# Kernel tuning notes

Hardware: AMD Instinct MI355X
Metric: run time of the kernel (lower is better)

## Reference

```python
import jax, jax.numpy as jnp
import numpy as np

N_NODES = 100000
SEQ = 16          # spiral length
IN_C = 3
NUM_CLASSES = 12


def _xavier(key, shape):
    fan_out, fan_in = shape
    limit = float(np.sqrt(6.0 / (fan_in + fan_out)))
    return jax.random.uniform(key, shape, jnp.float32, -limit, limit)


def setup_inputs() -> dict:
    key = jax.random.key(0)
    ks = jax.random.split(key, 8)
    x = jax.random.normal(ks[0], (N_NODES, IN_C), jnp.float32)
    indices = jax.random.randint(ks[1], (N_NODES, SEQ), 0, N_NODES, jnp.int64)
    return {
        "x": x,
        "indices": indices,
        "fc0_w": _xavier(ks[2], (16, IN_C)),
        "fc0_b": jnp.zeros((16,), jnp.float32),
        "w1": _xavier(ks[3], (32, 16 * SEQ)),
        "b1": jnp.zeros((32,), jnp.float32),
        "w2": _xavier(ks[4], (64, 32 * SEQ)),
        "b2": jnp.zeros((64,), jnp.float32),
        "w3": _xavier(ks[5], (128, 64 * SEQ)),
        "b3": jnp.zeros((128,), jnp.float32),
        "fc1_w": _xavier(ks[6], (256, 128)),
        "fc1_b": jnp.zeros((256,), jnp.float32),
        "fc2_w": _xavier(ks[7], (NUM_CLASSES, 256)),
        "fc2_b": jnp.zeros((NUM_CLASSES,), jnp.float32),
    }


def _spiral_conv(x, indices, w, b):
    # gather spiral neighborhoods: [N, S, C] -> [N, S*C], then linear
    n = indices.shape[0]
    g = x[indices.reshape(-1)].reshape(n, -1)
    return g @ w.T + b


def reference(x, indices, fc0_w, fc0_b, w1, b1, w2, b2, w3, b3,
              fc1_w, fc1_b, fc2_w, fc2_b):
    h = jax.nn.elu(x @ fc0_w.T + fc0_b)                 # [N, 16]
    h = jax.nn.elu(_spiral_conv(h, indices, w1, b1))    # [N, 32]
    h = jax.nn.elu(_spiral_conv(h, indices, w2, b2))    # [N, 64]
    h = jax.nn.elu(_spiral_conv(h, indices, w3, b3))    # [N, 128]
    h = jax.nn.elu(h @ fc1_w.T + fc1_b)                 # [N, 256]
    # dropout is identity in eval mode
    logits = h @ fc2_w.T + fc2_b                        # [N, num_classes]
    return jax.nn.log_softmax(logits, axis=1)
```

## Files before the change

### kernel.cpp

```cpp
#include <hip/hip_runtime.h>
#include <hip/hip_fp8.h>
#include <math.h>
#include <utility>


typedef __bf16 bf16x8 __attribute__((ext_vector_type(8)));
typedef float f32x16 __attribute__((ext_vector_type(16)));
typedef float f32x2 __attribute__((ext_vector_type(2)));

template <int V> using ic = std::integral_constant<int, V>;

template <typename F, int... Is>
__device__ __forceinline__ void static_for_impl(F&& f, std::integer_sequence<int, Is...>) {
    (f(ic<Is>{}), ...);
}
template <int N_, typename F>
__device__ __forceinline__ void static_for(F&& f) {
    static_for_impl(static_cast<F&&>(f), std::make_integer_sequence<int, N_>{});
}

template <int N_>
__device__ __forceinline__ void wait_vmcnt() {
    static_assert(N_ <= 63, "vmcnt range");
    __builtin_amdgcn_s_waitcnt((N_ & 0xF) | (0x7 << 4) | (0xF << 8) | ((N_ >> 4) << 14));
}

__device__ __forceinline__ void memfence_sched() { __builtin_amdgcn_sched_barrier(0x000F); }

__device__ __forceinline__ float elu_f(float v) { return v > 0.f ? v : expm1f(v); }

__device__ __forceinline__ unsigned char to_fp8(float v) {
    int p = __builtin_amdgcn_cvt_pk_fp8_f32(v, v, 0, false);
    return (unsigned char)p;
}

__device__ __forceinline__ unsigned int pk_bf16(float a, float b) {
    unsigned int r;
    asm("v_cvt_pk_bf16_f32 %0, %1, %2" : "=v"(r) : "v"(a), "v"(b));
    return r;
}

__device__ __forceinline__ bf16x8 dq8(long v) {
    unsigned int lo = (unsigned int)(unsigned long)v;
    unsigned int hi = (unsigned int)((unsigned long)v >> 32);
    f32x2 f0 = __builtin_amdgcn_cvt_pk_f32_fp8((int)lo, false);
    f32x2 f1 = __builtin_amdgcn_cvt_pk_f32_fp8((int)lo, true);
    f32x2 f2 = __builtin_amdgcn_cvt_pk_f32_fp8((int)hi, false);
    f32x2 f3 = __builtin_amdgcn_cvt_pk_f32_fp8((int)hi, true);
    union { unsigned int u[4]; bf16x8 b; } r;
    r.u[0] = pk_bf16(f0[0], f0[1]);
    r.u[1] = pk_bf16(f1[0], f1[1]);
    r.u[2] = pk_bf16(f2[0], f2[1]);
    r.u[3] = pk_bf16(f3[0], f3[1]);
    return r.b;
}

template <int K, int C>
__device__ __forceinline__ void swz_one(const float* __restrict__ src, __bf16* __restrict__ dst, int j)
{
    int col = j / K;
    int k = j & (K - 1);
    int chunk = ((k >> 6) * 8 + ((k & 63) >> 3)) * C + col;
    dst[chunk * 8 + (k & 7)] = (__bf16)src[j];
}

__global__ __launch_bounds__(256) void cvt_swz_kernel(const float* __restrict__ w1,
                                                      const float* __restrict__ w2,
                                                      const float* __restrict__ w3,
                                                      const float* __restrict__ f1,
                                                      const float* __restrict__ f2,
                                                      __bf16* __restrict__ d1,
                                                      __bf16* __restrict__ d2,
                                                      __bf16* __restrict__ d3,
                                                      __bf16* __restrict__ df1,
                                                      __bf16* __restrict__ df2p)
{
    int i = blockIdx.x * 256 + threadIdx.x;
    if (i < 8192)        swz_one<256, 32>(w1, d1, i);
    else if (i < 40960)  swz_one<512, 64>(w2, d2, i - 8192);
    else if (i < 172032) swz_one<1024, 128>(w3, d3, i - 40960);
    else if (i < 204800) swz_one<128, 256>(f1, df1, i - 172032);
    else if (i < 212992) {
        int d = i - 204800;
        int e = d & 7;
        int chunkIdx = d >> 3;
        int col = chunkIdx & 31;
        int q = chunkIdx >> 5;
        int k = (q >> 3) * 64 + (q & 7) * 8 + e;
        df2p[d] = (col < 12) ? (__bf16)f2[col * 256 + k] : (__bf16)0.f;
    }
}

__global__ __launch_bounds__(256) void idxT_kernel(const int* __restrict__ idx,
                                                   int* __restrict__ idxT, int N)
{
    int i = blockIdx.x * 256 + threadIdx.x;
    if (i >= N * 16) return;
    int n = i >> 4, s = i & 15;
    idxT[s * N + n] = idx[i];
}

__global__ __launch_bounds__(256) void fc0_kernel(const float* __restrict__ x,
                                                  const float* __restrict__ w,
                                                  const float* __restrict__ b,
                                                  __bf16* __restrict__ h0, int N)
{
    int n = blockIdx.x * 256 + threadIdx.x;
    if (n >= N) return;
    float x0 = x[n * 3 + 0], x1 = x[n * 3 + 1], x2 = x[n * 3 + 2];
    __bf16 ob[16];
#pragma unroll
    for (int j = 0; j < 16; ++j)
        ob[j] = (__bf16)elu_f(w[j * 3 + 0] * x0 + w[j * 3 + 1] * x1 + w[j * 3 + 2] * x2 + b[j]);
    int4* dst = (int4*)&h0[(size_t)n * 16];
    dst[0] = *(int4*)&ob[0];
    dst[1] = *(int4*)&ob[8];
}

template <int CIN, int S, int COUT_B, int COUT_TOT, int TILE_M, int RW, int CW,
          bool GATHER, bool OUTF8, int MINW, int NN>
__global__ __launch_bounds__(256, MINW) void mfma_layer(const __bf16* __restrict__ hin,
                                                        const int* __restrict__ idxT,
                                                        const __bf16* __restrict__ Wsw,
                                                        const float* __restrict__ bias,
                                                        void* __restrict__ hout)
{
    constexpr int K = CIN * S;
    constexpr int NSTEP = K / 64;
    static_assert(K % 64 == 0, "K%64");
    constexpr int WM = TILE_M / RW;
    constexpr int WN = COUT_B / CW;
    constexpr int MT = WM / 32;
    constexpr int NT = WN / 32;
    constexpr int IPS = GATHER ? (64 / CIN) : 1;
    constexpr int D = WM / 8;
    constexpr int Bn = NT * 4;
    constexpr int I = GATHER ? D : 0;
    constexpr int NBUFS = 3;
    static_assert(RW * CW == 4, "4 waves");
    static_assert(WM == 32 || WM == 64, "1-2 row subtiles per wave");

    constexpr int AB = 4 * NBUFS * WM * 128;
    constexpr int CB = OUTF8 ? TILE_M * (COUT_B + 16) : TILE_M * (COUT_B + 8) * 2;
    constexpr int SH = AB > CB ? AB : CB;
    __shared__ __align__(16) char smem[SH];

    const int tid = threadIdx.x;
    const int lane = tid & 63;
    const int w = tid >> 6;
    const int wr = w / CW;
    const int wc = w % CW;
    const int ml = lane & 31;
    const int kh = lane >> 5;
    const int m0 = blockIdx.x * TILE_M;
    const int col0 = blockIdx.y * COUT_B;
    const int rbase = m0 + wr * WM;

    char* const Aw = smem + w * (NBUFS * WM * 128);

    int ioff[GATHER ? D : 1];
    int koff[GATHER ? D : 1];
    int gmr[GATHER ? 1 : D];
    int coff[GATHER ? 1 : D];
#pragma unroll
    for (int i = 0; i < D; ++i) {
        int r = i * 8 + (lane >> 3);
        int c = (lane & 7) ^ (r & 7);
        int gm = rbase + r; if (gm >= NN) gm = NN - 1;
        if constexpr (GATHER) {
            ioff[i] = ((c * 8) / CIN) * NN + gm;
            koff[i] = (c * 8) & (CIN - 1);
        } else {
            gmr[i] = gm;
            coff[i] = c * 8;
        }
    }

    bf16x8 bfr[2][NT][4];
    int myIdx[GATHER ? 3 : 1][GATHER ? D : 1];

    const __bf16* wlane = Wsw + ((size_t)(col0 + wc * WN + ml) + (size_t)kh * COUT_TOT) * 8;

    auto loadB = [&](auto sc) {
        constexpr int s = decltype(sc)::value;
        if constexpr (s < NSTEP) {
#pragma unroll
            for (int ni = 0; ni < NT; ++ni)
#pragma unroll
                for (int ks = 0; ks < 4; ++ks)
                    bfr[s & 1][ni][ks] = *(const bf16x8*)(wlane
                        + (size_t)(s * 8 + ks * 2) * COUT_TOT * 8 + ni * 32 * 8);
        }
    };
    auto loadIdxS = [&](auto sc) {
        constexpr int s = decltype(sc)::value;
        if constexpr (GATHER && s < NSTEP) {
#pragma unroll
            for (int i = 0; i < D; ++i)
                myIdx[s % 3][i] = idxT[(s * IPS) * NN + ioff[i]];
        }
    };
    auto issueDMA = [&](auto sc) {
        constexpr int s = decltype(sc)::value;
        if constexpr (s < NSTEP) {
            char* base = Aw + (s % NBUFS) * (WM * 128);
#pragma unroll
            for (int i = 0; i < D; ++i) {
                const __bf16* src;
                if constexpr (GATHER)
                    src = hin + (size_t)myIdx[s % 3][i] * CIN + koff[i];
                else
                    src = hin + (size_t)gmr[i] * K + s * 64 + coff[i];
                __builtin_amdgcn_global_load_lds(
                    (const __attribute__((address_space(1))) void*)src,
                    (__attribute__((address_space(3))) void*)(base + i * 1024),
                    16, 0, 0);
            }
        }
    };

    f32x16 acc[MT][NT];
#pragma unroll
    for (int mi = 0; mi < MT; ++mi)
#pragma unroll
        for (int ni = 0; ni < NT; ++ni) { f32x16 z = {}; acc[mi][ni] = z; }

    loadIdxS(ic<0>{});
    loadIdxS(ic<1>{});
    loadIdxS(ic<2>{});
    memfence_sched();
    loadB(ic<0>{});
    memfence_sched();
    issueDMA(ic<0>{});
    memfence_sched();
    issueDMA(ic<1>{});
    memfence_sched();
    loadIdxS(ic<3>{});
    memfence_sched();

    static_for<NSTEP>([&](auto sc) {
        constexpr int s = decltype(sc)::value;
        constexpr int NW = D * (s + 1 < NSTEP) + I * (s + 3 < NSTEP);
        wait_vmcnt<NW>();
        memfence_sched();

        const char* base = Aw + (s % NBUFS) * (WM * 128);
        bf16x8 afr[MT][4];
#pragma unroll
        for (int mi = 0; mi < MT; ++mi)
#pragma unroll
            for (int ks = 0; ks < 4; ++ks) {
                int cb = ks * 2 + kh;
                afr[mi][ks] = *(const bf16x8*)(base + ((mi * 32 + ml) * 8 + (cb ^ (ml & 7))) * 16);
            }
        memfence_sched();

        loadB(ic<s + 1>{});
        memfence_sched();
        issueDMA(ic<s + 2>{});
        memfence_sched();
        loadIdxS(ic<s + 4>{});
        memfence_sched();

#pragma unroll
        for (int ks = 0; ks < 4; ++ks)
#pragma unroll
            for (int mi = 0; mi < MT; ++mi)
#pragma unroll
                for (int ni = 0; ni < NT; ++ni)
                    acc[mi][ni] = __builtin_amdgcn_mfma_f32_32x32x16_bf16(
                        afr[mi][ks], bfr[s & 1][ni][ks], acc[mi][ni], 0, 0, 0);
    });

    __syncthreads();
    if constexpr (OUTF8) {
        unsigned char* Cs8 = (unsigned char*)smem;
        constexpr int LDC8 = COUT_B + 16;
#pragma unroll
        for (int ni = 0; ni < NT; ++ni) {
            const int col = wc * WN + ni * 32 + ml;
            const float bv = bias[col0 + col];
#pragma unroll
            for (int mi = 0; mi < MT; ++mi) {
#pragma unroll
                for (int r = 0; r < 16; ++r) {
                    int row = wr * WM + mi * 32 + ((r & 3) + 8 * (r >> 2) + 4 * kh);
                    Cs8[row * LDC8 + col] = to_fp8(elu_f(acc[mi][ni][r] + bv));
                }
            }
        }
        __syncthreads();
        constexpr int C16 = COUT_B / 16;
#pragma unroll
        for (int j2 = tid; j2 < TILE_M * C16; j2 += 256) {
            int row = j2 / C16, c16 = j2 % C16;
            int gm = m0 + row;
            if (gm < NN)
                *(int4*)((unsigned char*)hout + (size_t)gm * COUT_TOT + col0 + c16 * 16)
                    = *(int4*)&Cs8[row * LDC8 + c16 * 16];
        }
    } else {
        __bf16* Cs = (__bf16*)smem;
        constexpr int LDC = COUT_B + 8;
#pragma unroll
        for (int ni = 0; ni < NT; ++ni) {
            const int col = wc * WN + ni * 32 + ml;
            const float bv = bias[col0 + col];
#pragma unroll
            for (int mi = 0; mi < MT; ++mi) {
#pragma unroll
                for (int r = 0; r < 16; ++r) {
                    int row = wr * WM + mi * 32 + ((r & 3) + 8 * (r >> 2) + 4 * kh);
                    Cs[row * LDC + col] = (__bf16)elu_f(acc[mi][ni][r] + bv);
                }
            }
        }
        __syncthreads();
        constexpr int C8 = COUT_B / 8;
#pragma unroll
        for (int j2 = tid; j2 < TILE_M * C8; j2 += 256) {
            int row = j2 / C8, c8 = j2 % C8;
            int gm = m0 + row;
            if (gm < NN)
                *(int4*)&((__bf16*)hout)[(size_t)gm * COUT_TOT + col0 + c8 * 8] = *(int4*)&Cs[row * LDC + c8 * 8];
        }
    }
}

__global__ __launch_bounds__(256, 3) void mfma3_mixed(const unsigned char* __restrict__ h2f8,
                                                      const int* __restrict__ idxT,
                                                      const __bf16* __restrict__ Wsw,
                                                      const float* __restrict__ bias,
                                                      __bf16* __restrict__ h3)
{
    constexpr int NN = 100000;
    constexpr int NSTEP = 16;
    constexpr int D = 2;
    constexpr int Bn = 8;
    constexpr int I = 2;
    constexpr int NBUFS = 3;
    __shared__ __align__(16) char smem[24576];

    const int tid = threadIdx.x;
    const int lane = tid & 63;
    const int w = tid >> 6;
    const int wr = w >> 1;
    const int wc = w & 1;
    const int ml = lane & 31;
    const int kh = lane >> 5;
    const int m0 = blockIdx.x * 64;
    const int rbase = m0 + wr * 32;

    char* const Aw = smem + w * (NBUFS * 2048);

    int ioff[D], koff[D];
#pragma unroll
    for (int i = 0; i < D; ++i) {
        int r = i * 16 + (lane >> 2);
        int c = (lane & 3) ^ (r & 3) ^ ((r >> 2) & 3);
        int gm = rbase + r; if (gm >= NN) gm = NN - 1;
        ioff[i] = gm;
        koff[i] = c * 16;
    }

    bf16x8 bfr[2][2][4];
    int myIdx[3][D];

    const __bf16* wlane = Wsw + ((size_t)(wc * 64 + ml) + (size_t)kh * 128) * 8;

    auto loadB = [&](auto sc) {
        constexpr int s = decltype(sc)::value;
        if constexpr (s < NSTEP) {
#pragma unroll
            for (int ni = 0; ni < 2; ++ni)
#pragma unroll
                for (int ks = 0; ks < 4; ++ks)
                    bfr[s & 1][ni][ks] = *(const bf16x8*)(wlane
                        + (size_t)(s * 8 + ks * 2) * 128 * 8 + ni * 32 * 8);
        }
    };
    auto loadIdxS = [&](auto sc) {
        constexpr int s = decltype(sc)::value;
        if constexpr (s < NSTEP) {
#pragma unroll
            for (int i = 0; i < D; ++i)
                myIdx[s % 3][i] = idxT[(size_t)s * NN + ioff[i]];
        }
    };
    auto issueDMA = [&](auto sc) {
        constexpr int s = decltype(sc)::value;
        if constexpr (s < NSTEP) {
            char* base = Aw + (s % NBUFS) * 2048;
#pragma unroll
            for (int i = 0; i < D; ++i) {
                const unsigned char* src = h2f8 + (size_t)myIdx[s % 3][i] * 64 + koff[i];
                __builtin_amdgcn_global_load_lds(
                    (const __attribute__((address_space(1))) void*)src,
                    (__attribute__((address_space(3))) void*)(base + i * 1024),
                    16, 0, 0);
            }
        }
    };

    f32x16 acc[2];
    { f32x16 z = {}; acc[0] = z; acc[1] = z; }

    loadIdxS(ic<0>{});
    loadIdxS(ic<1>{});
    loadIdxS(ic<2>{});
    memfence_sched();
    loadB(ic<0>{});
    memfence_sched();
    issueDMA(ic<0>{});
    memfence_sched();
    issueDMA(ic<1>{});
    memfence_sched();
    loadIdxS(ic<3>{});
    memfence_sched();

    static_for<NSTEP>([&](auto sc) {
        constexpr int s = decltype(sc)::value;
        constexpr int NW = (s == 0)
            ? (D * (1 < NSTEP) + I * (3 < NSTEP))
            : (I * (s + 2 < NSTEP) + Bn + D * (s + 1 < NSTEP) + I * (s + 3 < NSTEP));
        wait_vmcnt<NW>();
        memfence_sched();

        const char* base = Aw + (s % NBUFS) * 2048;
        long a8[4];
#pragma unroll
        for (int ks = 0; ks < 4; ++ks)
            a8[ks] = *(const long*)(base + ml * 64
                + (((ks ^ (ml & 3)) ^ ((ml >> 2) & 3)) << 4) + kh * 8);
        memfence_sched();

        loadB(ic<s + 1>{});
        memfence_sched();
        issueDMA(ic<s + 2>{});
        memfence_sched();
        loadIdxS(ic<s + 4>{});
        memfence_sched();

        bf16x8 afr[4];
#pragma unroll
        for (int ks = 0; ks < 4; ++ks)
            afr[ks] = dq8(a8[ks]);
#pragma unroll
        for (int ks = 0; ks < 4; ++ks)
#pragma unroll
            for (int ni = 0; ni < 2; ++ni)
                acc[ni] = __builtin_amdgcn_mfma_f32_32x32x16_bf16(
                    afr[ks], bfr[s & 1][ni][ks], acc[ni], 0, 0, 0);
    });

    __syncthreads();
    __bf16* Cs = (__bf16*)smem;
#pragma unroll
    for (int ni = 0; ni < 2; ++ni) {
        const int col = wc * 64 + ni * 32 + ml;
        const float bv = bias[col];
#pragma unroll
        for (int r = 0; r < 16; ++r) {
            int row = wr * 32 + ((r & 3) + 8 * (r >> 2) + 4 * kh);
            Cs[row * 136 + col] = (__bf16)elu_f(acc[ni][r] + bv);
        }
    }
    __syncthreads();
#pragma unroll
    for (int j2 = tid; j2 < 64 * 16; j2 += 256) {
        int row = j2 >> 4, c8 = j2 & 15;
        int gm = m0 + row;
        if (gm < NN)
            *(int4*)&h3[(size_t)gm * 128 + c8 * 8] = *(int4*)&Cs[row * 136 + c8 * 8];
    }
}

__global__ __launch_bounds__(256, 3) void fc12_kernel(const __bf16* __restrict__ h3,
                                                      const __bf16* __restrict__ Wsw,
                                                      const float* __restrict__ bias1,
                                                      const __bf16* __restrict__ W2p,
                                                      const float* __restrict__ bias2,
                                                      float* __restrict__ out)
{
    __shared__ __align__(16) char smem[32 * 264 * 2];
    const int tid = threadIdx.x;
    const int lane = tid & 63;
    const int w = tid >> 6;
    const int ml = lane & 31;
    const int kh = lane >> 5;
    const int m0 = blockIdx.x * 32;

    const __bf16* wlane = Wsw + ((size_t)(w * 64 + ml) + (size_t)kh * 256) * 8;
    bf16x8 bfr[2][2][4];
#pragma unroll
    for (int s = 0; s < 2; ++s)
#pragma unroll
        for (int ni = 0; ni < 2; ++ni)
#pragma unroll
            for (int ks = 0; ks < 4; ++ks)
                bfr[s][ni][ks] = *(const bf16x8*)(wlane
                    + (size_t)(s * 8 + ks * 2) * 256 * 8 + ni * 32 * 8);

    bf16x8 b2f[4];
#pragma unroll
    for (int ks = 0; ks < 4; ++ks)
        b2f[ks] = *(const bf16x8*)&W2p[((w * 8 + ks * 2 + kh) * 32 + ml) * 8];

#pragma unroll
    for (int t = 0; t < 2; ++t) {
        int j = w * 2 + t;
        int lr = j * 4 + (lane >> 4);
        int sc = (lane & 15) ^ (lr & 15);
        const __bf16* src = h3 + (size_t)(m0 + lr) * 128 + sc * 8;
        __builtin_amdgcn_global_load_lds(
            (const __attribute__((address_space(1))) void*)src,
            (__attribute__((address_space(3))) void*)(smem + j * 1024),
            16, 0, 0);
    }
    wait_vmcnt<0>();
    __syncthreads();

    f32x16 acc[2];
    { f32x16 z = {}; acc[0] = z; acc[1] = z; }
    const char* Ab = smem;
#pragma unroll
    for (int s = 0; s < 2; ++s) {
        bf16x8 afr[4];
#pragma unroll
        for (int ks = 0; ks < 4; ++ks) {
            int c16 = s * 8 + ks * 2 + kh;
            afr[ks] = *(const bf16x8*)(Ab + ml * 256 + ((c16 ^ (ml & 15)) * 16));
        }
#pragma unroll
        for (int ks = 0; ks < 4; ++ks)
#pragma unroll
            for (int ni = 0; ni < 2; ++ni)
                acc[ni] = __builtin_amdgcn_mfma_f32_32x32x16_bf16(afr[ks], bfr[s][ni][ks], acc[ni], 0, 0, 0);
    }
    __syncthreads();

    __bf16* Cs = (__bf16*)smem;
#pragma unroll
    for (int ni = 0; ni < 2; ++ni) {
        int col = w * 64 + ni * 32 + ml;
        float bv = bias1[col];
#pragma unroll
        for (int r = 0; r < 16; ++r) {
            int row = (r & 3) + 8 * (r >> 2) + 4 * kh;
            Cs[row * 264 + col] = (__bf16)elu_f(acc[ni][r] + bv);
        }
    }
    __syncthreads();

    bf16x8 a2[4];
#pragma unroll
    for (int ks = 0; ks < 4; ++ks)
        a2[ks] = *(const bf16x8*)&Cs[ml * 264 + w * 64 + ks * 16 + kh * 8];
    f32x16 acc2;
    { f32x16 z = {}; acc2 = z; }
#pragma unroll
    for (int ks = 0; ks < 4; ++ks)
        acc2 = __builtin_amdgcn_mfma_f32_32x32x16_bf16(a2[ks], b2f[ks], acc2, 0, 0, 0);
    __syncthreads();

    float* P = (float*)(smem + w * 4096);
#pragma unroll
    for (int r = 0; r < 16; ++r)
        P[((r & 3) + 8 * (r >> 2) + 4 * kh) * 32 + ml] = acc2[r];
    __syncthreads();

    float4 s4 = make_float4(0.f, 0.f, 0.f, 0.f);
#pragma unroll
    for (int pw = 0; pw < 4; ++pw) {
        float4 v = *(float4*)(smem + pw * 4096 + tid * 16);
        s4.x += v.x; s4.y += v.y; s4.z += v.z; s4.w += v.w;
    }
    __syncthreads();
    *(float4*)(smem + tid * 16) = s4;
    __syncthreads();

    if (tid < 32) {
        const float* L = (float*)smem + tid * 32;
        float logits[12], mx = -1e30f;
#pragma unroll
        for (int o = 0; o < 12; ++o) {
            logits[o] = L[o] + bias2[o];
            mx = fmaxf(mx, logits[o]);
        }
        float s = 0.f;
#pragma unroll
        for (int o = 0; o < 12; ++o) s += expf(logits[o] - mx);
        float lse = mx + logf(s);
        int n = m0 + tid;
        float4 o0 = make_float4(logits[0] - lse, logits[1] - lse, logits[2] - lse, logits[3] - lse);
        float4 o1 = make_float4(logits[4] - lse, logits[5] - lse, logits[6] - lse, logits[7] - lse);
        float4 o2 = make_float4(logits[8] - lse, logits[9] - lse, logits[10] - lse, logits[11] - lse);
        *(float4*)&out[(size_t)n * 12 + 0] = o0;
        *(float4*)&out[(size_t)n * 12 + 4] = o1;
        *(float4*)&out[(size_t)n * 12 + 8] = o2;
    }
}

extern "C" void kernel_launch(void* const* d_in, const int* in_sizes, int n_in,
                              void* d_out, int out_size, void* d_ws, size_t ws_size,
                              hipStream_t stream)
{
    const int N = 100000;
    const float* x     = (const float*)d_in[0];
    const int*   idx   = (const int*)  d_in[1];
    const float* fc0_w = (const float*)d_in[2];
    const float* fc0_b = (const float*)d_in[3];
    const float* w1    = (const float*)d_in[4];
    const float* b1    = (const float*)d_in[5];
    const float* w2    = (const float*)d_in[6];
    const float* b2    = (const float*)d_in[7];
    const float* w3    = (const float*)d_in[8];
    const float* b3    = (const float*)d_in[9];
    const float* fc1_w = (const float*)d_in[10];
    const float* fc1_b = (const float*)d_in[11];
    const float* fc2_w = (const float*)d_in[12];
    const float* fc2_b = (const float*)d_in[13];
    float* out = (float*)d_out;

    char* ws = (char*)d_ws;
    const int n_w1 = 32 * 256, n_w2 = 64 * 512, n_w3 = 128 * 1024, n_fc1 = 256 * 128;
    const int n_fc2p = 32 * 256;
    const int n_wb = n_w1 + n_w2 + n_w3 + n_fc1 + n_fc2p;
    __bf16* w1b = (__bf16*)ws;
    __bf16* w2b = w1b + n_w1;
    __bf16* w3b = w2b + n_w2;
    __bf16* f1b = w3b + n_w3;
    __bf16* f2b = f1b + n_fc1;
    size_t off = ((size_t)n_wb * 2 + 4095) & ~(size_t)4095;
    int* idxT = (int*)(ws + off);              off += (size_t)N * 16 * 4;
    __bf16* h0 = (__bf16*)(ws + off);          off += (size_t)N * 16 * 2;
    __bf16* h1 = (__bf16*)(ws + off);          off += (size_t)N * 32 * 2;
    unsigned char* h2f8 = (unsigned char*)(ws + off);  off += (size_t)N * 64;
    __bf16* h3 = (__bf16*)(ws + off);          off += (size_t)N * 128 * 2;

    cvt_swz_kernel<<<(n_wb + 255) / 256, 256, 0, stream>>>(w1, w2, w3, fc1_w, fc2_w,
                                                           w1b, w2b, w3b, f1b, f2b);
    idxT_kernel<<<(N * 16 + 255) / 256, 256, 0, stream>>>(idx, idxT, N);
    fc0_kernel<<<(N + 255) / 256, 256, 0, stream>>>(x, fc0_w, fc0_b, h0, N);

    mfma_layer<16, 16, 32, 32, 128, 4, 1, true, false, 3, 100000>
        <<<dim3((N + 127) / 128, 1), 256, 0, stream>>>(h0, idxT, w1b, b1, (void*)h1);
    mfma_layer<32, 16, 64, 64, 128, 4, 1, true, true, 3, 100000>
        <<<dim3((N + 127) / 128, 1), 256, 0, stream>>>(h1, idxT, w2b, b2, (void*)h2f8);
    mfma3_mixed<<<(N + 63) / 64, 256, 0, stream>>>(h2f8, idxT, w3b, b3, h3);
    fc12_kernel<<<N / 32, 256, 0, stream>>>(h3, f1b, fc1_b, f2b, fc2_b, out);
}
```

Before: 217.9 us.

## Merge prep kernels into one launch and process two row tiles per fc12 block

New measurement: 220.8 us. No clear change (+1.3%).

```diff
diff --git a/kernel.cpp b/kernel.cpp
--- a/kernel.cpp
+++ b/kernel.cpp
@@ -64,57 +64,60 @@
     dst[chunk * 8 + (k & 7)] = (__bf16)src[j];
 }
 
-__global__ __launch_bounds__(256) void cvt_swz_kernel(const float* __restrict__ w1,
-                                                      const float* __restrict__ w2,
-                                                      const float* __restrict__ w3,
-                                                      const float* __restrict__ f1,
-                                                      const float* __restrict__ f2,
-                                                      __bf16* __restrict__ d1,
-                                                      __bf16* __restrict__ d2,
-                                                      __bf16* __restrict__ d3,
-                                                      __bf16* __restrict__ df1,
-                                                      __bf16* __restrict__ df2p)
+__global__ __launch_bounds__(256) void prep_kernel(const float* __restrict__ w1,
+                                                   const float* __restrict__ w2,
+                                                   const float* __restrict__ w3,
+                                                   const float* __restrict__ f1,
+                                                   const float* __restrict__ f2,
+                                                   __bf16* __restrict__ d1,
+                                                   __bf16* __restrict__ d2,
+                                                   __bf16* __restrict__ d3,
+                                                   __bf16* __restrict__ df1,
+                                                   __bf16* __restrict__ df2p,
+                                                   const int* __restrict__ idx,
+                                                   int* __restrict__ idxT,
+                                                   const float* __restrict__ x,
+                                                   const float* __restrict__ fc0_w,
+                                                   const float* __restrict__ fc0_b,
+                                                   __bf16* __restrict__ h0,
+                                                   int N)
 {
-    int i = blockIdx.x * 256 + threadIdx.x;
-    if (i < 8192)        swz_one<256, 32>(w1, d1, i);
-    else if (i < 40960)  swz_one<512, 64>(w2, d2, i - 8192);
-    else if (i < 172032) swz_one<1024, 128>(w3, d3, i - 40960);
-    else if (i < 204800) swz_one<128, 256>(f1, df1, i - 172032);
-    else if (i < 212992) {
-        int d = i - 204800;
-        int e = d & 7;
-        int chunkIdx = d >> 3;
-        int col = chunkIdx & 31;
-        int q = chunkIdx >> 5;
-        int k = (q >> 3) * 64 + (q & 7) * 8 + e;
-        df2p[d] = (col < 12) ? (__bf16)f2[col * 256 + k] : (__bf16)0.f;
+    int b = blockIdx.x;
+    if (b < 832) {
+        int i = b * 256 + threadIdx.x;
+        if (i < 8192)        swz_one<256, 32>(w1, d1, i);
+        else if (i < 40960)  swz_one<512, 64>(w2, d2, i - 8192);
+        else if (i < 172032) swz_one<1024, 128>(w3, d3, i - 40960);
+        else if (i < 204800) swz_one<128, 256>(f1, df1, i - 172032);
+        else {
+            int d = i - 204800;
+            int e = d & 7;
+            int chunkIdx = d >> 3;
+            int col = chunkIdx & 31;
+            int q = chunkIdx >> 5;
+            int k = (q >> 3) * 64 + (q & 7) * 8 + e;
+            df2p[d] = (col < 12) ? (__bf16)f2[col * 256 + k] : (__bf16)0.f;
+        }
+    } else if (b < 7082) {
+        int i = (b - 832) * 256 + threadIdx.x;
+        if (i < N * 16) {
+            int n = i >> 4, s = i & 15;
+            idxT[s * N + n] = idx[i];
+        }
+    } else {
+        int n = (b - 7082) * 256 + threadIdx.x;
+        if (n < N) {
+            float x0 = x[n * 3 + 0], x1 = x[n * 3 + 1], x2 = x[n * 3 + 2];
+            __bf16 ob[16];
+#pragma unroll
+            for (int j = 0; j < 16; ++j)
+                ob[j] = (__bf16)elu_f(fc0_w[j * 3 + 0] * x0 + fc0_w[j * 3 + 1] * x1
+                                      + fc0_w[j * 3 + 2] * x2 + fc0_b[j]);
+            int4* dst = (int4*)&h0[(size_t)n * 16];
+            dst[0] = *(int4*)&ob[0];
+            dst[1] = *(int4*)&ob[8];
+        }
     }
-}
-
-__global__ __launch_bounds__(256) void idxT_kernel(const int* __restrict__ idx,
-                                                   int* __restrict__ idxT, int N)
-{
-    int i = blockIdx.x * 256 + threadIdx.x;
-    if (i >= N * 16) return;
-    int n = i >> 4, s = i & 15;
-    idxT[s * N + n] = idx[i];
-}
-
-__global__ __launch_bounds__(256) void fc0_kernel(const float* __restrict__ x,
-                                                  const float* __restrict__ w,
-                                                  const float* __restrict__ b,
-                                                  __bf16* __restrict__ h0, int N)
-{
-    int n = blockIdx.x * 256 + threadIdx.x;
-    if (n >= N) return;
-    float x0 = x[n * 3 + 0], x1 = x[n * 3 + 1], x2 = x[n * 3 + 2];
-    __bf16 ob[16];
-#pragma unroll
-    for (int j = 0; j < 16; ++j)
-        ob[j] = (__bf16)elu_f(w[j * 3 + 0] * x0 + w[j * 3 + 1] * x1 + w[j * 3 + 2] * x2 + b[j]);
-    int4* dst = (int4*)&h0[(size_t)n * 16];
-    dst[0] = *(int4*)&ob[0];
-    dst[1] = *(int4*)&ob[8];
 }
 
 template <int CIN, int S, int COUT_B, int COUT_TOT, int TILE_M, int RW, int CW,
@@ -480,7 +483,8 @@
                                                       const float* __restrict__ bias1,
                                                       const __bf16* __restrict__ W2p,
                                                       const float* __restrict__ bias2,
-                                                      float* __restrict__ out)
+                                                      float* __restrict__ out,
+                                                      int N)
 {
     __shared__ __align__(16) char smem[32 * 264 * 2];
     const int tid = threadIdx.x;
@@ -488,7 +492,7 @@
     const int w = tid >> 6;
     const int ml = lane & 31;
     const int kh = lane >> 5;
-    const int m0 = blockIdx.x * 32;
+    const int m0 = blockIdx.x * 64;
 
     const __bf16* wlane = Wsw + ((size_t)(w * 64 + ml) + (size_t)kh * 256) * 8;
     bf16x8 bfr[2][2][4];
@@ -507,97 +511,104 @@
         b2f[ks] = *(const bf16x8*)&W2p[((w * 8 + ks * 2 + kh) * 32 + ml) * 8];
 
 #pragma unroll
-    for (int t = 0; t < 2; ++t) {
-        int j = w * 2 + t;
-        int lr = j * 4 + (lane >> 4);
-        int sc = (lane & 15) ^ (lr & 15);
-        const __bf16* src = h3 + (size_t)(m0 + lr) * 128 + sc * 8;
-        __builtin_amdgcn_global_load_lds(
-            (const __attribute__((address_space(1))) void*)src,
-            (__attribute__((address_space(3))) void*)(smem + j * 1024),
-            16, 0, 0);
-    }
-    wait_vmcnt<0>();
-    __syncthreads();
-
-    f32x16 acc[2];
-    { f32x16 z = {}; acc[0] = z; acc[1] = z; }
-    const char* Ab = smem;
-#pragma unroll
-    for (int s = 0; s < 2; ++s) {
-        bf16x8 afr[4];
-#pragma unroll
-        for (int ks = 0; ks < 4; ++ks) {
-            int c16 = s * 8 + ks * 2 + kh;
-            afr[ks] = *(const bf16x8*)(Ab + ml * 256 + ((c16 ^ (ml & 15)) * 16));
-        }
+    for (int half = 0; half < 2; ++half) {
+        const int mb = m0 + half * 32;
+        if (mb >= N) break;
+        if (half) __syncthreads();
+
+#pragma unroll
+        for (int t = 0; t < 2; ++t) {
+            int j = w * 2 + t;
+            int lr = j * 4 + (lane >> 4);
+            int sc = (lane & 15) ^ (lr & 15);
+            const __bf16* src = h3 + (size_t)(mb + lr) * 128 + sc * 8;
+            __builtin_amdgcn_global_load_lds(
+                (const __attribute__((address_space(1))) void*)src,
+                (__attribute__((address_space(3))) void*)(smem + j * 1024),
+                16, 0, 0);
+        }
+        wait_vmcnt<0>();
+        __syncthreads();
+
+        f32x16 acc[2];
+        { f32x16 z = {}; acc[0] = z; acc[1] = z; }
+        const char* Ab = smem;
+#pragma unroll
+        for (int s = 0; s < 2; ++s) {
+            bf16x8 afr[4];
+#pragma unroll
+            for (int ks = 0; ks < 4; ++ks) {
+                int c16 = s * 8 + ks * 2 + kh;
+                afr[ks] = *(const bf16x8*)(Ab + ml * 256 + ((c16 ^ (ml & 15)) * 16));
+            }
+#pragma unroll
+            for (int ks = 0; ks < 4; ++ks)
+#pragma unroll
+                for (int ni = 0; ni < 2; ++ni)
+                    acc[ni] = __builtin_amdgcn_mfma_f32_32x32x16_bf16(afr[ks], bfr[s][ni][ks], acc[ni], 0, 0, 0);
+        }
+        __syncthreads();
+
+        __bf16* Cs = (__bf16*)smem;
+#pragma unroll
+        for (int ni = 0; ni < 2; ++ni) {
+            int col = w * 64 + ni * 32 + ml;
+            float bv = bias1[col];
+#pragma unroll
+            for (int r = 0; r < 16; ++r) {
+                int row = (r & 3) + 8 * (r >> 2) + 4 * kh;
+                Cs[row * 264 + col] = (__bf16)elu_f(acc[ni][r] + bv);
+            }
+        }
+        __syncthreads();
+
+        bf16x8 a2[4];
 #pragma unroll
         for (int ks = 0; ks < 4; ++ks)
-#pragma unroll
-            for (int ni = 0; ni < 2; ++ni)
-                acc[ni] = __builtin_amdgcn_mfma_f32_32x32x16_bf16(afr[ks], bfr[s][ni][ks], acc[ni], 0, 0, 0);
-    }
-    __syncthreads();
-
-    __bf16* Cs = (__bf16*)smem;
-#pragma unroll
-    for (int ni = 0; ni < 2; ++ni) {
-        int col = w * 64 + ni * 32 + ml;
-        float bv = bias1[col];
-#pragma unroll
-        for (int r = 0; r < 16; ++r) {
-            int row = (r & 3) + 8 * (r >> 2) + 4 * kh;
-            Cs[row * 264 + col] = (__bf16)elu_f(acc[ni][r] + bv);
-        }
-    }
-    __syncthreads();
-
-    bf16x8 a2[4];
-#pragma unroll
-    for (int ks = 0; ks < 4; ++ks)
-        a2[ks] = *(const bf16x8*)&Cs[ml * 264 + w * 64 + ks * 16 + kh * 8];
-    f32x16 acc2;
-    { f32x16 z = {}; acc2 = z; }
-#pragma unroll
-    for (int ks = 0; ks < 4; ++ks)
-        acc2 = __builtin_amdgcn_mfma_f32_32x32x16_bf16(a2[ks], b2f[ks], acc2, 0, 0, 0);
-    __syncthreads();
-
-    float* P = (float*)(smem + w * 4096);
-#pragma unroll
-    for (int r = 0; r < 16; ++r)
-        P[((r & 3) + 8 * (r >> 2) + 4 * kh) * 32 + ml] = acc2[r];
-    __syncthreads();
-
-    float4 s4 = make_float4(0.f, 0.f, 0.f, 0.f);
-#pragma unroll
-    for (int pw = 0; pw < 4; ++pw) {
-        float4 v = *(float4*)(smem + pw * 4096 + tid * 16);
-        s4.x += v.x; s4.y += v.y; s4.z += v.z; s4.w += v.w;
-    }
-    __syncthreads();
-    *(float4*)(smem + tid * 16) = s4;
-    __syncthreads();
-
-    if (tid < 32) {
-        const float* L = (float*)smem + tid * 32;
-        float logits[12], mx = -1e30f;
-#pragma unroll
-        for (int o = 0; o < 12; ++o) {
-            logits[o] = L[o] + bias2[o];
-            mx = fmaxf(mx, logits[o]);
-        }
-        float s = 0.f;
-#pragma unroll
-        for (int o = 0; o < 12; ++o) s += expf(logits[o] - mx);
-        float lse = mx + logf(s);
-        int n = m0 + tid;
-        float4 o0 = make_float4(logits[0] - lse, logits[1] - lse, logits[2] - lse, logits[3] - lse);
-        float4 o1 = make_float4(logits[4] - lse, logits[5] - lse, logits[6] - lse, logits[7] - lse);
-        float4 o2 = make_float4(logits[8] - lse, logits[9] - lse, logits[10] - lse, logits[11] - lse);
-        *(float4*)&out[(size_t)n * 12 + 0] = o0;
-        *(float4*)&out[(size_t)n * 12 + 4] = o1;
-        *(float4*)&out[(size_t)n * 12 + 8] = o2;
+            a2[ks] = *(const bf16x8*)&Cs[ml * 264 + w * 64 + ks * 16 + kh * 8];
+        f32x16 acc2;
+        { f32x16 z = {}; acc2 = z; }
+#pragma unroll
+        for (int ks = 0; ks < 4; ++ks)
+            acc2 = __builtin_amdgcn_mfma_f32_32x32x16_bf16(a2[ks], b2f[ks], acc2, 0, 0, 0);
+        __syncthreads();
+
+        float* P = (float*)(smem + w * 4096);
+#pragma unroll
+        for (int r = 0; r < 16; ++r)
+            P[((r & 3) + 8 * (r >> 2) + 4 * kh) * 32 + ml] = acc2[r];
+        __syncthreads();
+
+        float4 s4 = make_float4(0.f, 0.f, 0.f, 0.f);
+#pragma unroll
+        for (int pw = 0; pw < 4; ++pw) {
+            float4 v = *(float4*)(smem + pw * 4096 + tid * 16);
+            s4.x += v.x; s4.y += v.y; s4.z += v.z; s4.w += v.w;
+        }
+        __syncthreads();
+        *(float4*)(smem + tid * 16) = s4;
+        __syncthreads();
+
+        if (tid < 32) {
+            const float* L = (float*)smem + tid * 32;
+            float logits[12], mx = -1e30f;
+#pragma unroll
+            for (int o = 0; o < 12; ++o) {
+                logits[o] = L[o] + bias2[o];
+                mx = fmaxf(mx, logits[o]);
+            }
+            float s = 0.f;
+#pragma unroll
+            for (int o = 0; o < 12; ++o) s += expf(logits[o] - mx);
+            float lse = mx + logf(s);
+            int n = mb + tid;
+            float4 o0 = make_float4(logits[0] - lse, logits[1] - lse, logits[2] - lse, logits[3] - lse);
+            float4 o1 = make_float4(logits[4] - lse, logits[5] - lse, logits[6] - lse, logits[7] - lse);
+            float4 o2 = make_float4(logits[8] - lse, logits[9] - lse, logits[10] - lse, logits[11] - lse);
+            *(float4*)&out[(size_t)n * 12 + 0] = o0;
+            *(float4*)&out[(size_t)n * 12 + 4] = o1;
+            *(float4*)&out[(size_t)n * 12 + 8] = o2;
+        }
     }
 }
 
@@ -638,15 +649,14 @@
     unsigned char* h2f8 = (unsigned char*)(ws + off);  off += (size_t)N * 64;
     __bf16* h3 = (__bf16*)(ws + off);          off += (size_t)N * 128 * 2;
 
-    cvt_swz_kernel<<<(n_wb + 255) / 256, 256, 0, stream>>>(w1, w2, w3, fc1_w, fc2_w,
-                                                           w1b, w2b, w3b, f1b, f2b);
-    idxT_kernel<<<(N * 16 + 255) / 256, 256, 0, stream>>>(idx, idxT, N);
-    fc0_kernel<<<(N + 255) / 256, 256, 0, stream>>>(x, fc0_w, fc0_b, h0, N);
+    prep_kernel<<<7473, 256, 0, stream>>>(w1, w2, w3, fc1_w, fc2_w,
+                                          w1b, w2b, w3b, f1b, f2b,
+                                          idx, idxT, x, fc0_w, fc0_b, h0, N);
 
     mfma_layer<16, 16, 32, 32, 128, 4, 1, true, false, 3, 100000>
         <<<dim3((N + 127) / 128, 1), 256, 0, stream>>>(h0, idxT, w1b, b1, (void*)h1);
     mfma_layer<32, 16, 64, 64, 128, 4, 1, true, true, 3, 100000>
         <<<dim3((N + 127) / 128, 1), 256, 0, stream>>>(h1, idxT, w2b, b2, (void*)h2f8);
     mfma3_mixed<<<(N + 63) / 64, 256, 0, stream>>>(h2f8, idxT, w3b, b3, h3);
-    fc12_kernel<<<N / 32, 256, 0, stream>>>(h3, f1b, fc1_b, f2b, fc2_b, out);
-}
+    fc12_kernel<<<(N + 63) / 64, 256, 0, stream>>>(h3, f1b, fc1_b, f2b, fc2_b, out, N);
+}
```
